# Performance work log

Measured on AMD Instinct MI355X. Metric: run time of the kernel, lower is better.

## Reference

```python
import jax, jax.numpy as jnp
import numpy as np

EPS = 1e-5
B, NA, T, D, H, L, DFF, E = 4, 64, 128, 128, 8, 3, 512, 65536
NN = T * NA  # nodes per graph = t*n after reshape(b, t*n, f)
DH = D // H


def _layer_norm(x, g, b):
    m = x.mean(-1, keepdims=True)
    v = ((x - m) ** 2).mean(-1, keepdims=True)
    return (x - m) * jax.lax.rsqrt(v + EPS) * g + b


def _pos_encoding(t, d):
    pos = jnp.arange(t, dtype=jnp.float32)[:, None]
    i = jnp.arange(0, d, 2, dtype=jnp.float32)
    ang = pos * jnp.exp(-jnp.log(10000.0) * i / d)
    pe = jnp.zeros((t, d), jnp.float32)
    return pe.at[:, 0::2].set(jnp.sin(ang)).at[:, 1::2].set(jnp.cos(ang))


def _forward(all_hist_feat, edge_weight, hist_w, hist_b,
             attn_wq, attn_bq, attn_wk, attn_bk, attn_wv, attn_bv, attn_wo, attn_bo,
             ln1_g, ln1_b, ff_w1, ff_b1, ff_w2, ff_b2, ln2_g, ln2_b,
             bn_g, bn_b, lin_graph_w, lin_graph_b, edge_index):
    b, n, t, _ = all_hist_feat.shape
    # history embedding: Linear(3, D)  -> [b, n, t, D]
    x = all_hist_feat @ hist_w + hist_b
    # sinusoidal positional encoding over the time axis
    out_e = x + _pos_encoding(t, D)
    scale = 1.0 / jnp.sqrt(jnp.asarray(DH, jnp.float32))
    for l in range(L):  # small fixed layer count
        q = out_e @ attn_wq[l] + attn_bq[l]
        k = out_e @ attn_wk[l] + attn_bk[l]
        v = out_e @ attn_wv[l] + attn_bv[l]
        qh = q.reshape(b, n, t, H, DH)
        kh = k.reshape(b, n, t, H, DH)
        vh = v.reshape(b, n, t, H, DH)
        scores = jnp.einsum('bnqhd,bnkhd->bnhqk', qh, kh) * scale
        attn = jax.nn.softmax(scores, axis=-1)
        o = jnp.einsum('bnhqk,bnkhd->bnqhd', attn, vh).reshape(b, n, t, D)
        o = o @ attn_wo[l] + attn_bo[l]
        h1 = _layer_norm(out_e + o, ln1_g[l], ln1_b[l])
        ff = jax.nn.relu(h1 @ ff_w1[l] + ff_b1[l]) @ ff_w2[l] + ff_b2[l]
        out_e = _layer_norm(h1 + ff, ln2_g[l], ln2_b[l])
    # graph stage: nodes are (time, agent) pairs, index = time*n + agent
    graph_w = out_e.transpose(0, 2, 1, 3).reshape(b, t * n, D)
    graph_x = x.transpose(0, 2, 1, 3).reshape(b, t * n, D)
    # GCNConv_Fixed_W (no self loops, no normalize): per-node score then
    # edge-weighted scatter-add from source to target (PyG convention)
    s = (graph_w * graph_x).sum(-1)  # [b, t*n]
    src, dst = edge_index[:, 0], edge_index[:, 1]

    def agg(s_b, src_b, dst_b, ew_b):
        return jax.ops.segment_sum(ew_b * s_b[src_b], dst_b, num_segments=NN)

    graph_out = jax.vmap(agg)(s, src, dst, edge_weight)  # [b, t*n]
    g = graph_out.reshape(b, t, n)
    # BatchNorm2d(1) on [b, 1, n, t]: single channel -> global batch stats
    m = g.mean()
    var = g.var()
    g = (g - m) * jax.lax.rsqrt(var + EPS) * bn_g[0] + bn_b[0]
    g4 = g.transpose(0, 2, 1)[..., None]  # [b, n, t, 1]
    return g4 @ lin_graph_w + lin_graph_b  # [b, n, t, D]


def setup_inputs() -> dict:
    keys = iter(jax.random.split(jax.random.key(0), 64))

    def nrm(shape, scale):
        return jax.random.normal(next(keys), shape, jnp.float32) * scale

    inp = {
        'all_hist_feat': nrm((B, NA, T, 3), 1.0),
        'edge_index': jax.random.randint(next(keys), (B, 2, E), 0, NN, jnp.int32),
        'edge_weight': jax.random.uniform(next(keys), (B, E), jnp.float32),
        'hist_w': nrm((3, D), 0.5), 'hist_b': nrm((D,), 0.02),
        'attn_wq': nrm((L, D, D), D ** -0.5), 'attn_bq': jnp.zeros((L, D)),
        'attn_wk': nrm((L, D, D), D ** -0.5), 'attn_bk': jnp.zeros((L, D)),
        'attn_wv': nrm((L, D, D), D ** -0.5), 'attn_bv': jnp.zeros((L, D)),
        'attn_wo': nrm((L, D, D), D ** -0.5), 'attn_bo': jnp.zeros((L, D)),
        'ln1_g': jnp.ones((L, D)), 'ln1_b': jnp.zeros((L, D)),
        'ff_w1': nrm((L, D, DFF), D ** -0.5), 'ff_b1': jnp.zeros((L, DFF)),
        'ff_w2': nrm((L, DFF, D), DFF ** -0.5), 'ff_b2': jnp.zeros((L, D)),
        'ln2_g': jnp.ones((L, D)), 'ln2_b': jnp.zeros((L, D)),
        'bn_g': jnp.ones((1,)), 'bn_b': jnp.zeros((1,)),
        'lin_graph_w': nrm((1, D), 1.0), 'lin_graph_b': jnp.zeros((D,)),
    }
    return inp


def reference(all_hist_feat, edge_index, edge_weight, hist_w, hist_b,
              attn_wq, attn_bq, attn_wk, attn_bk, attn_wv, attn_bv, attn_wo, attn_bo,
              ln1_g, ln1_b, ff_w1, ff_b1, ff_w2, ff_b2, ln2_g, ln2_b,
              bn_g, bn_b, lin_graph_w, lin_graph_b):
    return _forward(all_hist_feat, edge_weight, hist_w, hist_b,
                    attn_wq, attn_bq, attn_wk, attn_bk, attn_wv, attn_bv, attn_wo, attn_bo,
                    ln1_g, ln1_b, ff_w1, ff_b1, ff_w2, ff_b2, ln2_g, ln2_b,
                    bn_g, bn_b, lin_graph_w, lin_graph_b, edge_index)
```

## Files before the change

### kernel.cpp

```cpp
#include <hip/hip_runtime.h>
#include <hip/hip_bf16.h>
#include <math.h>

#define EPS_ 1e-5f
constexpr int B_ = 4, NA = 64, T_ = 128, D_ = 128, H_ = 8, L_ = 3, DFF = 512, E_ = 65536;
constexpr int DH = D_ / H_;
constexpr int NN = T_ * NA;
constexpr int NTOT = B_ * NA * T_;
constexpr int QLD = 384;
constexpr size_t NE_ = (size_t)NTOT * D_;

typedef __bf16 bf16x8 __attribute__((ext_vector_type(8)));
typedef float f32x4 __attribute__((ext_vector_type(4)));

__global__ __launch_bounds__(256) void embed_kernel(
    const float* __restrict__ hist, const float* __restrict__ w,
    const float* __restrict__ b, float* __restrict__ x, float* __restrict__ e) {
  int idx = blockIdx.x * 256 + threadIdx.x;
  if (idx >= NTOT * D_) return;
  int d = idx & (D_ - 1);
  int r = idx >> 7;
  int t = r & (T_ - 1);
  const float* hp = hist + (size_t)r * 3;
  float acc = b[d];
  acc += hp[0] * w[0 * D_ + d];
  acc += hp[1] * w[1 * D_ + d];
  acc += hp[2] * w[2 * D_ + d];
  x[idx] = acc;
  int p = d >> 1;
  float ang = (float)t * expf(-logf(10000.f) * (2.f * (float)p) / (float)D_);
  float pe = (d & 1) ? cosf(ang) : sinf(ang);
  e[idx] = acc + pe;
}

__global__ __launch_bounds__(256) void convert_weights(
    const float* __restrict__ wq, const float* __restrict__ wk,
    const float* __restrict__ wv, const float* __restrict__ wo,
    const float* __restrict__ w1, const float* __restrict__ w2,
    __bf16* __restrict__ hi, __bf16* __restrict__ lo) {
  const int LW = 196608;
  int idx = blockIdx.x * 256 + threadIdx.x;
  if (idx >= L_ * LW) return;
  int l = idx / LW;
  int rem = idx - l * LW;
  float src;
  int n, k, K, segoff;
  if (rem < 49152) {
    n = rem >> 7; k = rem & 127; K = 128; segoff = 0;
    int which = n >> 7, nl = n & 127;
    const float* W = (which == 0) ? wq : (which == 1) ? wk : wv;
    src = W[(size_t)l * 16384 + k * 128 + nl];
  } else if (rem < 65536) {
    int r2 = rem - 49152;
    n = r2 >> 7; k = r2 & 127; K = 128; segoff = 49152;
    src = wo[(size_t)l * 16384 + k * 128 + n];
  } else if (rem < 131072) {
    int r2 = rem - 65536;
    n = r2 >> 7; k = r2 & 127; K = 128; segoff = 65536;
    src = w1[(size_t)l * 65536 + k * 512 + n];
  } else {
    int r2 = rem - 131072;
    n = r2 >> 9; k = r2 & 511; K = 512; segoff = 131072;
    src = w2[(size_t)l * 65536 + k * 128 + n];
  }
  int nt = n >> 4, kt = k >> 5;
  int lane = ((k >> 3) & 3) * 16 + (n & 15);
  int j = k & 7;
  int dst = l * LW + segoff + ((nt * (K / 32) + kt) * 64 + lane) * 8 + j;
  __bf16 h = (__bf16)src;
  hi[dst] = h;
  lo[dst] = (__bf16)(src - (float)h);
}

__global__ __launch_bounds__(256) void bias_pack(
    const float* __restrict__ bq, const float* __restrict__ bk,
    const float* __restrict__ bv, float* __restrict__ pb) {
  int idx = blockIdx.x * 256 + threadIdx.x;
  if (idx >= L_ * QLD) return;
  int l = idx / QLD, n = idx - l * QLD;
  int which = n >> 7, nl = n & 127;
  const float* src = (which == 0) ? bq : (which == 1) ? bk : bv;
  pb[idx] = src[l * 128 + nl];
}

__device__ __forceinline__ void split8(const float* __restrict__ p,
                                       bf16x8& hi, bf16x8& lo) {
  float4 x0 = *(const float4*)p;
  float4 x1 = *(const float4*)(p + 4);
  float xv[8] = {x0.x, x0.y, x0.z, x0.w, x1.x, x1.y, x1.z, x1.w};
#pragma unroll
  for (int j = 0; j < 8; ++j) {
    __bf16 h = (__bf16)xv[j];
    hi[j] = h;
    lo[j] = (__bf16)(xv[j] - (float)h);
  }
}

__device__ __forceinline__ void cvt8(const float4& x0, const float4& x1,
                                     bf16x8& hi, bf16x8& lo) {
  float xv[8] = {x0.x, x0.y, x0.z, x0.w, x1.x, x1.y, x1.z, x1.w};
#pragma unroll
  for (int j = 0; j < 8; ++j) {
    __bf16 h = (__bf16)xv[j];
    hi[j] = h;
    lo[j] = (__bf16)(xv[j] - (float)h);
  }
}

#define GB_LOADA(buf, kt)                                                                  \
  {                                                                                        \
    _Pragma("unroll") for (int mf_ = 0; mf_ < 4; ++mf_) {                                  \
      const float* p_ = A + (size_t)(row0 + mf_ * 16 + m16) * lda + (kt) * 32 + quad * 8;  \
      ar[buf][mf_][0] = *(const float4*)p_;                                                \
      ar[buf][mf_][1] = *(const float4*)(p_ + 4);                                          \
    }                                                                                      \
  }
#define GB_LOADW(buf, kt)                                                                  \
  {                                                                                        \
    _Pragma("unroll") for (int nf_ = 0; nf_ < 4; ++nf_) {                                  \
      size_t off_ = ((size_t)(ctb + nf_) * (K / 32) + (kt)) * 512 + lane * 8;              \
      bh[buf][nf_] = *(const bf16x8*)(Whi + off_);                                         \
      bl[buf][nf_] = *(const bf16x8*)(Wlo + off_);                                         \
    }                                                                                      \
  }

template <int EPI, int K>
__global__ __launch_bounds__(256) void gemm_big(
    const float* __restrict__ A, int lda,
    const __bf16* __restrict__ Whi, const __bf16* __restrict__ Wlo,
    const float* __restrict__ bias,
    float* __restrict__ C, int ldc) {
  const int wave = threadIdx.x >> 6;
  const int lane = threadIdx.x & 63;
  const int m16 = lane & 15;
  const int quad = lane >> 4;
  const int wrow = wave >> 1, wcol = wave & 1;
  const int row0 = blockIdx.y * 128 + wrow * 64;
  const int col0 = blockIdx.x * 128 + wcol * 64;
  const int ctb = col0 >> 4;

  f32x4 acc[4][4] = {};
  float4 ar[2][4][2];
  bf16x8 bh[2][4], bl[2][4];
  GB_LOADA(0, 0);
  GB_LOADW(0, 0);
#pragma unroll
  for (int kt = 0; kt < K / 32; ++kt) {
    const int cur = kt & 1, nxt = cur ^ 1;
    if (kt < K / 32 - 1) {
      GB_LOADA(nxt, kt + 1);
      GB_LOADW(nxt, kt + 1);
    }
    bf16x8 ahi[4], alo[4];
#pragma unroll
    for (int mf = 0; mf < 4; ++mf)
      cvt8(ar[cur][mf][0], ar[cur][mf][1], ahi[mf], alo[mf]);
#pragma unroll
    for (int mf = 0; mf < 4; ++mf)
#pragma unroll
      for (int nf = 0; nf < 4; ++nf) {
        acc[mf][nf] = __builtin_amdgcn_mfma_f32_16x16x32_bf16(ahi[mf], bh[cur][nf], acc[mf][nf], 0, 0, 0);
        acc[mf][nf] = __builtin_amdgcn_mfma_f32_16x16x32_bf16(ahi[mf], bl[cur][nf], acc[mf][nf], 0, 0, 0);
        acc[mf][nf] = __builtin_amdgcn_mfma_f32_16x16x32_bf16(alo[mf], bh[cur][nf], acc[mf][nf], 0, 0, 0);
      }
  }
#pragma unroll
  for (int mf = 0; mf < 4; ++mf)
#pragma unroll
    for (int nf = 0; nf < 4; ++nf) {
      int c = col0 + nf * 16 + m16;
      float bj = bias[c];
#pragma unroll
      for (int reg = 0; reg < 4; ++reg) {
        int r = row0 + mf * 16 + quad * 4 + reg;
        float v = acc[mf][nf][reg] + bj;
        if (EPI == 1) v = fmaxf(v, 0.f);
        C[(size_t)r * ldc + c] = v;
      }
    }
}
#undef GB_LOADA
#undef GB_LOADW

template <int K>
__global__ __launch_bounds__(256) void gemm_ln(
    const float* __restrict__ A, int lda,
    const __bf16* __restrict__ Whi, const __bf16* __restrict__ Wlo,
    const float* __restrict__ bias, const float* __restrict__ resid,
    const float* __restrict__ lng, const float* __restrict__ lnb,
    float* __restrict__ C) {
  const int wave = threadIdx.x >> 6;
  const int lane = threadIdx.x & 63;
  const int m16 = lane & 15;
  const int quad = lane >> 4;
  const int wrow = wave >> 1, wcol = wave & 1;
  const int row0 = blockIdx.y * 64 + wrow * 32;
  const int col0 = wcol * 64;
  const int ctb = wcol * 4;

  f32x4 acc[2][4] = {};
#pragma unroll
  for (int k0 = 0; k0 < K; k0 += 32) {
    bf16x8 ahi[2], alo[2];
#pragma unroll
    for (int mf = 0; mf < 2; ++mf)
      split8(A + (size_t)(row0 + mf * 16 + m16) * lda + k0 + quad * 8, ahi[mf], alo[mf]);
    bf16x8 bhi[4], blo[4];
#pragma unroll
    for (int nf = 0; nf < 4; ++nf) {
      size_t off = ((size_t)(ctb + nf) * (K / 32) + (k0 >> 5)) * 512 + lane * 8;
      bhi[nf] = *(const bf16x8*)(Whi + off);
      blo[nf] = *(const bf16x8*)(Wlo + off);
    }
#pragma unroll
    for (int mf = 0; mf < 2; ++mf)
#pragma unroll
      for (int nf = 0; nf < 4; ++nf) {
        acc[mf][nf] = __builtin_amdgcn_mfma_f32_16x16x32_bf16(ahi[mf], bhi[nf], acc[mf][nf], 0, 0, 0);
        acc[mf][nf] = __builtin_amdgcn_mfma_f32_16x16x32_bf16(ahi[mf], blo[nf], acc[mf][nf], 0, 0, 0);
        acc[mf][nf] = __builtin_amdgcn_mfma_f32_16x16x32_bf16(alo[mf], bhi[nf], acc[mf][nf], 0, 0, 0);
      }
  }
  __shared__ float rs[64][2], rq[64][2];
#pragma unroll
  for (int mf = 0; mf < 2; ++mf)
#pragma unroll
    for (int reg = 0; reg < 4; ++reg) {
      int lr = wrow * 32 + mf * 16 + quad * 4 + reg;
      int gr = blockIdx.y * 64 + lr;
      float s = 0.f, qq = 0.f;
#pragma unroll
      for (int nf = 0; nf < 4; ++nf) {
        int c = col0 + nf * 16 + m16;
        float v = acc[mf][nf][reg] + bias[c] + resid[(size_t)gr * 128 + c];
        acc[mf][nf][reg] = v;
        s += v;
        qq += v * v;
      }
#pragma unroll
      for (int off = 1; off < 16; off <<= 1) {
        s += __shfl_xor(s, off, 64);
        qq += __shfl_xor(qq, off, 64);
      }
      if (m16 == 0) { rs[lr][wcol] = s; rq[lr][wcol] = qq; }
    }
  __syncthreads();
#pragma unroll
  for (int mf = 0; mf < 2; ++mf)
#pragma unroll
    for (int reg = 0; reg < 4; ++reg) {
      int lr = wrow * 32 + mf * 16 + quad * 4 + reg;
      int gr = blockIdx.y * 64 + lr;
      float mean = (rs[lr][0] + rs[lr][1]) * (1.f / 128.f);
      float var = (rq[lr][0] + rq[lr][1]) * (1.f / 128.f) - mean * mean;
      float rstd = rsqrtf(var + EPS_);
#pragma unroll
      for (int nf = 0; nf < 4; ++nf) {
        int c = col0 + nf * 16 + m16;
        C[(size_t)gr * 128 + c] = (acc[mf][nf][reg] - mean) * rstd * lng[c] + lnb[c];
      }
    }
}

#define FF1_LOADA(buf, kt)                                                                  \
  {                                                                                         \
    _Pragma("unroll") for (int mf_ = 0; mf_ < 2; ++mf_) {                                   \
      const float* p_ = A + (size_t)(grow0 + mf_ * 16 + m16) * 128 + (kt) * 32 + quad * 8;  \
      ar[buf][mf_][0] = *(const float4*)p_;                                                 \
      ar[buf][mf_][1] = *(const float4*)(p_ + 4);                                           \
    }                                                                                       \
  }
#define FF1_LOADW(buf, kt)                                                                  \
  {                                                                                         \
    _Pragma("unroll") for (int nf_ = 0; nf_ < 8; ++nf_) {                                   \
      size_t off_ = ((size_t)(wave * 8 + nf_) * 4 + (kt)) * 512 + lane * 8;                 \
      bh[buf][nf_] = *(const bf16x8*)(W1hi + off_);                                         \
      bl[buf][nf_] = *(const bf16x8*)(W1lo + off_);                                         \
    }                                                                                       \
  }
#define FF2_LOADW(buf, kt)                                                                  \
  {                                                                                         \
    _Pragma("unroll") for (int nf_ = 0; nf_ < 2; ++nf_) {                                   \
      size_t off_ = ((size_t)(wave * 2 + nf_) * 16 + (kt)) * 512 + lane * 8;                \
      wh[buf][nf_] = *(const bf16x8*)(W2hi + off_);                                         \
      wl[buf][nf_] = *(const bf16x8*)(W2lo + off_);                                         \
    }                                                                                       \
  }

template <int SDOT>
__global__ __launch_bounds__(256) void ff_fused(
    const float* __restrict__ A,
    const __bf16* __restrict__ W1hi, const __bf16* __restrict__ W1lo,
    const float* __restrict__ b1v,
    const __bf16* __restrict__ W2hi, const __bf16* __restrict__ W2lo,
    const float* __restrict__ b2v, const float* __restrict__ resid,
    const float* __restrict__ lng, const float* __restrict__ lnb,
    float* __restrict__ C,
    const float* __restrict__ bx, float* __restrict__ sdst) {
  extern __shared__ float Amid[];
  const int wave = threadIdx.x >> 6;
  const int lane = threadIdx.x & 63;
  const int m16 = lane & 15;
  const int quad = lane >> 4;
  const int grow0 = blockIdx.x * 32;

  {
    f32x4 acc[2][8] = {};
    float4 ar[2][2][2];
    bf16x8 bh[2][8], bl[2][8];
    FF1_LOADA(0, 0);
    FF1_LOADW(0, 0);
#pragma unroll
    for (int kt = 0; kt < 4; ++kt) {
      const int cur = kt & 1, nxt = cur ^ 1;
      if (kt < 3) {
        FF1_LOADA(nxt, kt + 1);
        FF1_LOADW(nxt, kt + 1);
      }
      bf16x8 ahi[2], alo[2];
#pragma unroll
      for (int mf = 0; mf < 2; ++mf)
        cvt8(ar[cur][mf][0], ar[cur][mf][1], ahi[mf], alo[mf]);
#pragma unroll
      for (int nf = 0; nf < 8; ++nf)
#pragma unroll
        for (int mf = 0; mf < 2; ++mf) {
          acc[mf][nf] = __builtin_amdgcn_mfma_f32_16x16x32_bf16(ahi[mf], bh[cur][nf], acc[mf][nf], 0, 0, 0);
          acc[mf][nf] = __builtin_amdgcn_mfma_f32_16x16x32_bf16(ahi[mf], bl[cur][nf], acc[mf][nf], 0, 0, 0);
          acc[mf][nf] = __builtin_amdgcn_mfma_f32_16x16x32_bf16(alo[mf], bh[cur][nf], acc[mf][nf], 0, 0, 0);
        }
    }
#pragma unroll
    for (int mf = 0; mf < 2; ++mf)
#pragma unroll
      for (int nf = 0; nf < 8; ++nf) {
        int c = wave * 128 + nf * 16 + m16;
        float bj = b1v[c];
#pragma unroll
        for (int reg = 0; reg < 4; ++reg) {
          int r = mf * 16 + quad * 4 + reg;
          Amid[r * 513 + c] = fmaxf(acc[mf][nf][reg] + bj, 0.f);
        }
      }
  }
  __syncthreads();

  f32x4 acc2[2][2] = {};
  {
    bf16x8 wh[2][2], wl[2][2];
    FF2_LOADW(0, 0);
#pragma unroll
    for (int kt = 0; kt < 16; ++kt) {
      const int cur = kt & 1;
      if (kt < 15) FF2_LOADW(cur ^ 1, kt + 1);
      bf16x8 ahi[2], alo[2];
#pragma unroll
      for (int mf = 0; mf < 2; ++mf)
        split8(&Amid[(mf * 16 + m16) * 513 + kt * 32 + quad * 8], ahi[mf], alo[mf]);
#pragma unroll
      for (int mf = 0; mf < 2; ++mf)
#pragma unroll
        for (int nf = 0; nf < 2; ++nf) {
          acc2[mf][nf] = __builtin_amdgcn_mfma_f32_16x16x32_bf16(ahi[mf], wh[cur][nf], acc2[mf][nf], 0, 0, 0);
          acc2[mf][nf] = __builtin_amdgcn_mfma_f32_16x16x32_bf16(ahi[mf], wl[cur][nf], acc2[mf][nf], 0, 0, 0);
          acc2[mf][nf] = __builtin_amdgcn_mfma_f32_16x16x32_bf16(alo[mf], wh[cur][nf], acc2[mf][nf], 0, 0, 0);
        }
    }
  }

  __shared__ float rs[32][4], rq[32][4], sd[32][4];
  const int col0 = wave * 32;
#pragma unroll
  for (int mf = 0; mf < 2; ++mf)
#pragma unroll
    for (int reg = 0; reg < 4; ++reg) {
      int lr = mf * 16 + quad * 4 + reg;
      int gr = grow0 + lr;
      float s = 0.f, qq = 0.f;
#pragma unroll
      for (int nf = 0; nf < 2; ++nf) {
        int c = col0 + nf * 16 + m16;
        float v = acc2[mf][nf][reg] + b2v[c] + resid[(size_t)gr * 128 + c];
        acc2[mf][nf][reg] = v;
        s += v;
        qq += v * v;
      }
#pragma unroll
      for (int off = 1; off < 16; off <<= 1) {
        s += __shfl_xor(s, off, 64);
        qq += __shfl_xor(qq, off, 64);
      }
      if (m16 == 0) { rs[lr][wave] = s; rq[lr][wave] = qq; }
    }
  __syncthreads();
#pragma unroll
  for (int mf = 0; mf < 2; ++mf)
#pragma unroll
    for (int reg = 0; reg < 4; ++reg) {
      int lr = mf * 16 + quad * 4 + reg;
      int gr = grow0 + lr;
      float mean = (rs[lr][0] + rs[lr][1] + rs[lr][2] + rs[lr][3]) * (1.f / 128.f);
      float var = (rq[lr][0] + rq[lr][1] + rq[lr][2] + rq[lr][3]) * (1.f / 128.f) - mean * mean;
      float rstd = rsqrtf(var + EPS_);
      float sdp = 0.f;
#pragma unroll
      for (int nf = 0; nf < 2; ++nf) {
        int c = col0 + nf * 16 + m16;
        float v = (acc2[mf][nf][reg] - mean) * rstd * lng[c] + lnb[c];
        C[(size_t)gr * 128 + c] = v;
        if (SDOT) sdp += v * bx[(size_t)gr * 128 + c];
      }
      if (SDOT) {
#pragma unroll
        for (int off = 1; off < 16; off <<= 1) sdp += __shfl_xor(sdp, off, 64);
        if (m16 == 0) sd[lr][wave] = sdp;
      }
    }
  if (SDOT) {
    __syncthreads();
    if (threadIdx.x < 32) {
      int lr = threadIdx.x;
      int gr = grow0 + lr;
      float sv = sd[lr][0] + sd[lr][1] + sd[lr][2] + sd[lr][3];
      int t = gr & (T_ - 1);
      int bn = gr >> 7;
      int n = bn & (NA - 1);
      int b = bn >> 6;
      sdst[(size_t)b * NN + t * NA + n] = sv;
    }
  }
}
#undef FF1_LOADA
#undef FF1_LOADW
#undef FF2_LOADW

__global__ __launch_bounds__(256) void attn_mfma(float* __restrict__ qkv) {
  const int h = blockIdx.x & (H_ - 1);
  const int bn = blockIdx.x >> 3;
  const int wave = threadIdx.x >> 6;
  const int lane = threadIdx.x & 63;
  const int m16 = lane & 15;
  const int quad = lane >> 4;
  const int row0 = wave * 32;
  const float* Qb = qkv + (size_t)bn * T_ * QLD + h * DH;
  const float* Kb = Qb + 128;
  const float* Vb = Qb + 256;
  float* Ob = (float*)Vb;

  __shared__ __bf16 Plds[4][32][136];
  __shared__ __bf16 KH[8][32][8], KL[8][32][8];
  __shared__ __bf16 VH[4][64][8], VL[4][64][8];

  for (int u = threadIdx.x; u < 1024; u += 256) {
    int isV = u >> 9;
    int r2 = u & 511;
    int t = r2 >> 2, c4 = r2 & 3;
    float4 v = *(const float4*)((isV ? Vb : Kb) + (size_t)t * QLD + c4 * 4);
    float xv[4] = {v.x, v.y, v.z, v.w};
#pragma unroll
    for (int i = 0; i < 4; ++i) {
      int dh = c4 * 4 + i;
      __bf16 hh = (__bf16)xv[i];
      __bf16 ll = (__bf16)(xv[i] - (float)hh);
      if (isV) {
        int kc = t >> 5, rem = t & 31;
        int vl = (rem >> 3) * 16 + dh;
        VH[kc][vl][rem & 7] = hh;
        VL[kc][vl][rem & 7] = ll;
      } else {
        int nf = t >> 4;
        int kl = (dh >> 3) * 16 + (t & 15);
        KH[nf][kl][dh & 7] = hh;
        KL[nf][kl][dh & 7] = ll;
      }
    }
  }

  bf16x8 qhi[2], qlo[2];
#pragma unroll
  for (int mf = 0; mf < 2; ++mf) {
    if (quad < 2) {
      split8(Qb + (size_t)(row0 + mf * 16 + m16) * QLD + quad * 8, qhi[mf], qlo[mf]);
    } else {
#pragma unroll
      for (int j = 0; j < 8; ++j) { qhi[mf][j] = (__bf16)0.f; qlo[mf][j] = (__bf16)0.f; }
    }
  }
  __syncthreads();

  f32x4 acc[2][8] = {};
#pragma unroll
  for (int nf = 0; nf < 8; ++nf) {
    bf16x8 khi, klo;
    if (quad < 2) {
      khi = *(const bf16x8*)&KH[nf][lane][0];
      klo = *(const bf16x8*)&KL[nf][lane][0];
    } else {
#pragma unroll
      for (int j = 0; j < 8; ++j) { khi[j] = (__bf16)0.f; klo[j] = (__bf16)0.f; }
    }
#pragma unroll
    for (int mf = 0; mf < 2; ++mf) {
      acc[mf][nf] = __builtin_amdgcn_mfma_f32_16x16x32_bf16(qhi[mf], khi, acc[mf][nf], 0, 0, 0);
      acc[mf][nf] = __builtin_amdgcn_mfma_f32_16x16x32_bf16(qhi[mf], klo, acc[mf][nf], 0, 0, 0);
      acc[mf][nf] = __builtin_amdgcn_mfma_f32_16x16x32_bf16(qlo[mf], khi, acc[mf][nf], 0, 0, 0);
    }
  }

  const float scale = 0.25f;
#pragma unroll
  for (int mf = 0; mf < 2; ++mf)
#pragma unroll
    for (int reg = 0; reg < 4; ++reg) {
      float mx = -1e30f;
#pragma unroll
      for (int nf = 0; nf < 8; ++nf) mx = fmaxf(mx, acc[mf][nf][reg]);
#pragma unroll
      for (int off = 1; off < 16; off <<= 1) mx = fmaxf(mx, __shfl_xor(mx, off, 64));
      float sum = 0.f;
#pragma unroll
      for (int nf = 0; nf < 8; ++nf) {
        float e = __expf((acc[mf][nf][reg] - mx) * scale);
        acc[mf][nf][reg] = e;
        sum += e;
      }
#pragma unroll
      for (int off = 1; off < 16; off <<= 1) sum += __shfl_xor(sum, off, 64);
      float inv = 1.f / sum;
#pragma unroll
      for (int nf = 0; nf < 8; ++nf) acc[mf][nf][reg] *= inv;
    }

#pragma unroll
  for (int mf = 0; mf < 2; ++mf)
#pragma unroll
    for (int nf = 0; nf < 8; ++nf)
#pragma unroll
      for (int reg = 0; reg < 4; ++reg)
        Plds[wave][mf * 16 + quad * 4 + reg][nf * 16 + m16] = (__bf16)acc[mf][nf][reg];

  f32x4 oacc[2] = {};
#pragma unroll
  for (int kc = 0; kc < 4; ++kc) {
    bf16x8 pa0 = *(const bf16x8*)&Plds[wave][m16][kc * 32 + quad * 8];
    bf16x8 pa1 = *(const bf16x8*)&Plds[wave][16 + m16][kc * 32 + quad * 8];
    bf16x8 vhi = *(const bf16x8*)&VH[kc][lane][0];
    bf16x8 vlo = *(const bf16x8*)&VL[kc][lane][0];
    oacc[0] = __builtin_amdgcn_mfma_f32_16x16x32_bf16(pa0, vhi, oacc[0], 0, 0, 0);
    oacc[0] = __builtin_amdgcn_mfma_f32_16x16x32_bf16(pa0, vlo, oacc[0], 0, 0, 0);
    oacc[1] = __builtin_amdgcn_mfma_f32_16x16x32_bf16(pa1, vhi, oacc[1], 0, 0, 0);
    oacc[1] = __builtin_amdgcn_mfma_f32_16x16x32_bf16(pa1, vlo, oacc[1], 0, 0, 0);
  }

#pragma unroll
  for (int mf = 0; mf < 2; ++mf)
#pragma unroll
    for (int reg = 0; reg < 4; ++reg) {
      int r = row0 + mf * 16 + quad * 4 + reg;
      Ob[(size_t)r * QLD + m16] = oacc[mf][reg];
    }
}

__global__ __launch_bounds__(256) void scatter_kernel(
    const float* __restrict__ s, const int* __restrict__ ei,
    const float* __restrict__ ew, float* __restrict__ g) {
  int idx = blockIdx.x * 256 + threadIdx.x;
  if (idx >= B_ * E_) return;
  int b = idx >> 16;
  int e = idx & (E_ - 1);
  int src = ei[(size_t)b * 2 * E_ + e];
  int dst = ei[(size_t)b * 2 * E_ + E_ + e];
  float w = ew[(size_t)b * E_ + e];
  atomicAdd(&g[(size_t)b * NN + dst], w * s[(size_t)b * NN + src]);
}

__global__ __launch_bounds__(256) void stats_partial(
    const float* __restrict__ g, float* __restrict__ st) {
  int i = blockIdx.x * 256 + threadIdx.x;
  float v = g[i];
  float sum = v, sq = v * v;
#pragma unroll
  for (int off = 32; off; off >>= 1) {
    sum += __shfl_down(sum, off, 64);
    sq += __shfl_down(sq, off, 64);
  }
  __shared__ float s1[4], s2[4];
  int w = threadIdx.x >> 6;
  if ((threadIdx.x & 63) == 0) { s1[w] = sum; s2[w] = sq; }
  __syncthreads();
  if (threadIdx.x == 0) {
    atomicAdd(&st[0], s1[0] + s1[1] + s1[2] + s1[3]);
    atomicAdd(&st[1], s2[0] + s2[1] + s2[2] + s2[3]);
  }
}

__global__ __launch_bounds__(256) void final_kernel(
    const float* __restrict__ g, const float* __restrict__ st,
    const float* __restrict__ bng, const float* __restrict__ bnb,
    const float* __restrict__ lw, const float* __restrict__ lb,
    float* __restrict__ out) {
  int idx = blockIdx.x * 256 + threadIdx.x;
  if (idx >= NTOT * D_) return;
  int d = idx & (D_ - 1);
  int r = idx >> 7;
  int t = r & (T_ - 1);
  int bn = r >> 7;
  int n = bn & (NA - 1);
  int b = bn >> 6;
  const float invn = 1.f / (float)(B_ * NN);
  float m = st[0] * invn;
  float var = st[1] * invn - m * m;
  float rs = rsqrtf(var + EPS_);
  float gv = g[(size_t)b * NN + t * NA + n];
  float val = (gv - m) * rs * bng[0] + bnb[0];
  out[idx] = val * lw[d] + lb[d];
}

extern "C" void kernel_launch(void* const* d_in, const int* in_sizes, int n_in,
                              void* d_out, int out_size, void* d_ws, size_t ws_size,
                              hipStream_t stream) {
  const float* hist = (const float*)d_in[0];
  const int* eidx = (const int*)d_in[1];
  const float* ew = (const float*)d_in[2];
  const float* hw = (const float*)d_in[3];
  const float* hb = (const float*)d_in[4];
  const float* wq = (const float*)d_in[5];
  const float* bq = (const float*)d_in[6];
  const float* wk = (const float*)d_in[7];
  const float* bk = (const float*)d_in[8];
  const float* wv = (const float*)d_in[9];
  const float* bv = (const float*)d_in[10];
  const float* wo = (const float*)d_in[11];
  const float* bo = (const float*)d_in[12];
  const float* ln1g = (const float*)d_in[13];
  const float* ln1b = (const float*)d_in[14];
  const float* w1 = (const float*)d_in[15];
  const float* b1 = (const float*)d_in[16];
  const float* w2 = (const float*)d_in[17];
  const float* b2 = (const float*)d_in[18];
  const float* ln2g = (const float*)d_in[19];
  const float* ln2b = (const float*)d_in[20];
  const float* bng = (const float*)d_in[21];
  const float* bnb = (const float*)d_in[22];
  const float* lgw = (const float*)d_in[23];
  const float* lgb = (const float*)d_in[24];
  float* out = (float*)d_out;

  float* ws = (float*)d_ws;
  const size_t NE = NE_;
  float* bx = ws + 0 * NE;
  float* be = ws + 1 * NE;
  float* h1 = ws + 2 * NE;
  float* qkv = ws + 3 * NE;
  float* bs_ = ws + 7 * NE;
  float* bg_ = bs_ + NTOT;
  float* bst = bg_ + NTOT;
  float* pbias = bst + 2;
  const int LW = 196608;
  __bf16* whiB = (__bf16*)(pbias + L_ * QLD);
  __bf16* wloB = whiB + (size_t)L_ * LW;

  const size_t ffshm = (size_t)32 * 513 * sizeof(float);
  static bool ff_attr_done = false;
  if (!ff_attr_done) {
    (void)hipFuncSetAttribute(reinterpret_cast<const void*>(&ff_fused<0>),
                              hipFuncAttributeMaxDynamicSharedMemorySize, (int)ffshm);
    (void)hipFuncSetAttribute(reinterpret_cast<const void*>(&ff_fused<1>),
                              hipFuncAttributeMaxDynamicSharedMemorySize, (int)ffshm);
    ff_attr_done = true;
  }

  convert_weights<<<(L_ * LW + 255) / 256, 256, 0, stream>>>(
      wq, wk, wv, wo, w1, w2, whiB, wloB);
  bias_pack<<<(L_ * QLD + 255) / 256, 256, 0, stream>>>(bq, bk, bv, pbias);
  embed_kernel<<<(NTOT * D_) / 256, 256, 0, stream>>>(hist, hw, hb, bx, be);

  for (int l = 0; l < L_; ++l) {
    const __bf16* hiL = whiB + (size_t)l * LW;
    const __bf16* loL = wloB + (size_t)l * LW;
    gemm_big<0, 128><<<dim3(3, NTOT / 128), 256, 0, stream>>>(
        be, 128, hiL, loL, pbias + l * QLD, qkv, QLD);
    attn_mfma<<<B_ * NA * H_, 256, 0, stream>>>(qkv);
    gemm_ln<128><<<dim3(1, NTOT / 64), 256, 0, stream>>>(
        qkv + 256, QLD, hiL + 49152, loL + 49152, bo + l * D_, be,
        ln1g + l * D_, ln1b + l * D_, h1);
    if (l < L_ - 1) {
      ff_fused<0><<<NTOT / 32, 256, ffshm, stream>>>(
          h1, hiL + 65536, loL + 65536, b1 + l * DFF,
          hiL + 131072, loL + 131072, b2 + l * D_, h1,
          ln2g + l * D_, ln2b + l * D_, be, nullptr, nullptr);
    } else {
      ff_fused<1><<<NTOT / 32, 256, ffshm, stream>>>(
          h1, hiL + 65536, loL + 65536, b1 + l * DFF,
          hiL + 131072, loL + 131072, b2 + l * D_, h1,
          ln2g + l * D_, ln2b + l * D_, be, bx, bs_);
    }
  }

  hipMemsetAsync(bg_, 0, ((size_t)B_ * NN + 2) * sizeof(float), stream);
  scatter_kernel<<<(B_ * E_) / 256, 256, 0, stream>>>(bs_, eidx, ew, bg_);
  stats_partial<<<(B_ * NN) / 256, 256, 0, stream>>>(bg_, bst);
  final_kernel<<<(NTOT * D_) / 256, 256, 0, stream>>>(bg_, bst, bng, bnb, lgw, lgb, out);
}
```

Measured before the change: 550.2 us.

## Retile fused FFN to 64-row blocks with 8 waves and pre-split bf16 intermediate

The fused feed-forward kernel now processes 64 rows per block with 512 threads (8 waves). Each wave owns 64 hidden columns in the first GEMM and 16 output columns in the second, so each weight fragment is reused across more rows. The ReLU intermediate is stored in shared memory already split into packed bf16 hi/lo pairs, which removes the repeated fp32-to-bf16 splitting during the second GEMM. The A-operand loads are no longer double-buffered, and the larger shared-memory footprint per block may lower occupancy.

```diff
diff --git a/kernel.cpp b/kernel.cpp
--- a/kernel.cpp
+++ b/kernel.cpp
@@ -11,6 +11,7 @@
 constexpr size_t NE_ = (size_t)NTOT * D_;
 
 typedef __bf16 bf16x8 __attribute__((ext_vector_type(8)));
+typedef __bf16 bf16x2 __attribute__((ext_vector_type(2)));
 typedef float f32x4 __attribute__((ext_vector_type(4)));
 
 __global__ __launch_bounds__(256) void embed_kernel(
@@ -107,6 +108,26 @@
   }
 }
 
+__device__ __forceinline__ unsigned pack_hl(float v) {
+  __bf16 h = (__bf16)v;
+  __bf16 l = (__bf16)(v - (float)h);
+  bf16x2 p;
+  p[0] = h;
+  p[1] = l;
+  return __builtin_bit_cast(unsigned, p);
+}
+
+__device__ __forceinline__ void unpack8(const uint4& a, const uint4& b,
+                                        bf16x8& hi, bf16x8& lo) {
+  unsigned w[8] = {a.x, a.y, a.z, a.w, b.x, b.y, b.z, b.w};
+#pragma unroll
+  for (int j = 0; j < 8; ++j) {
+    bf16x2 p = __builtin_bit_cast(bf16x2, w[j]);
+    hi[j] = p[0];
+    lo[j] = p[1];
+  }
+}
+
 #define GB_LOADA(buf, kt)                                                                  \
   {                                                                                        \
     _Pragma("unroll") for (int mf_ = 0; mf_ < 4; ++mf_) {                                  \
@@ -262,33 +283,23 @@
     }
 }
 
-#define FF1_LOADA(buf, kt)                                                                  \
-  {                                                                                         \
-    _Pragma("unroll") for (int mf_ = 0; mf_ < 2; ++mf_) {                                   \
-      const float* p_ = A + (size_t)(grow0 + mf_ * 16 + m16) * 128 + (kt) * 32 + quad * 8;  \
-      ar[buf][mf_][0] = *(const float4*)p_;                                                 \
-      ar[buf][mf_][1] = *(const float4*)(p_ + 4);                                           \
-    }                                                                                       \
-  }
 #define FF1_LOADW(buf, kt)                                                                  \
   {                                                                                         \
-    _Pragma("unroll") for (int nf_ = 0; nf_ < 8; ++nf_) {                                   \
-      size_t off_ = ((size_t)(wave * 8 + nf_) * 4 + (kt)) * 512 + lane * 8;                 \
+    _Pragma("unroll") for (int nf_ = 0; nf_ < 4; ++nf_) {                                   \
+      size_t off_ = ((size_t)(wave * 4 + nf_) * 4 + (kt)) * 512 + lane * 8;                 \
       bh[buf][nf_] = *(const bf16x8*)(W1hi + off_);                                         \
       bl[buf][nf_] = *(const bf16x8*)(W1lo + off_);                                         \
     }                                                                                       \
   }
 #define FF2_LOADW(buf, kt)                                                                  \
   {                                                                                         \
-    _Pragma("unroll") for (int nf_ = 0; nf_ < 2; ++nf_) {                                   \
-      size_t off_ = ((size_t)(wave * 2 + nf_) * 16 + (kt)) * 512 + lane * 8;                \
-      wh[buf][nf_] = *(const bf16x8*)(W2hi + off_);                                         \
-      wl[buf][nf_] = *(const bf16x8*)(W2lo + off_);                                         \
-    }                                                                                       \
+    size_t off_ = ((size_t)wave * 16 + (kt)) * 512 + lane * 8;                              \
+    wh[buf] = *(const bf16x8*)(W2hi + off_);                                                \
+    wl[buf] = *(const bf16x8*)(W2lo + off_);                                                \
   }
 
 template <int SDOT>
-__global__ __launch_bounds__(256) void ff_fused(
+__global__ __launch_bounds__(512) void ff_fused(
     const float* __restrict__ A,
     const __bf16* __restrict__ W1hi, const __bf16* __restrict__ W1lo,
     const float* __restrict__ b1v,
@@ -297,94 +308,82 @@
     const float* __restrict__ lng, const float* __restrict__ lnb,
     float* __restrict__ C,
     const float* __restrict__ bx, float* __restrict__ sdst) {
-  extern __shared__ float Amid[];
+  extern __shared__ unsigned AmidU[];
   const int wave = threadIdx.x >> 6;
   const int lane = threadIdx.x & 63;
   const int m16 = lane & 15;
   const int quad = lane >> 4;
-  const int grow0 = blockIdx.x * 32;
+  const int grow0 = blockIdx.x * 64;
 
   {
-    f32x4 acc[2][8] = {};
-    float4 ar[2][2][2];
-    bf16x8 bh[2][8], bl[2][8];
-    FF1_LOADA(0, 0);
+    f32x4 acc[4][4] = {};
+    bf16x8 bh[2][4], bl[2][4];
     FF1_LOADW(0, 0);
 #pragma unroll
     for (int kt = 0; kt < 4; ++kt) {
-      const int cur = kt & 1, nxt = cur ^ 1;
-      if (kt < 3) {
-        FF1_LOADA(nxt, kt + 1);
-        FF1_LOADW(nxt, kt + 1);
-      }
-      bf16x8 ahi[2], alo[2];
-#pragma unroll
-      for (int mf = 0; mf < 2; ++mf)
-        cvt8(ar[cur][mf][0], ar[cur][mf][1], ahi[mf], alo[mf]);
-#pragma unroll
-      for (int nf = 0; nf < 8; ++nf)
-#pragma unroll
-        for (int mf = 0; mf < 2; ++mf) {
+      const int cur = kt & 1;
+      if (kt < 3) FF1_LOADW(cur ^ 1, kt + 1);
+      bf16x8 ahi[4], alo[4];
+#pragma unroll
+      for (int mf = 0; mf < 4; ++mf)
+        split8(A + (size_t)(grow0 + mf * 16 + m16) * 128 + kt * 32 + quad * 8, ahi[mf], alo[mf]);
+#pragma unroll
+      for (int mf = 0; mf < 4; ++mf)
+#pragma unroll
+        for (int nf = 0; nf < 4; ++nf) {
           acc[mf][nf] = __builtin_amdgcn_mfma_f32_16x16x32_bf16(ahi[mf], bh[cur][nf], acc[mf][nf], 0, 0, 0);
           acc[mf][nf] = __builtin_amdgcn_mfma_f32_16x16x32_bf16(ahi[mf], bl[cur][nf], acc[mf][nf], 0, 0, 0);
           acc[mf][nf] = __builtin_amdgcn_mfma_f32_16x16x32_bf16(alo[mf], bh[cur][nf], acc[mf][nf], 0, 0, 0);
         }
     }
 #pragma unroll
-    for (int mf = 0; mf < 2; ++mf)
-#pragma unroll
-      for (int nf = 0; nf < 8; ++nf) {
-        int c = wave * 128 + nf * 16 + m16;
+    for (int mf = 0; mf < 4; ++mf)
+#pragma unroll
+      for (int nf = 0; nf < 4; ++nf) {
+        int c = wave * 64 + nf * 16 + m16;
         float bj = b1v[c];
 #pragma unroll
         for (int reg = 0; reg < 4; ++reg) {
           int r = mf * 16 + quad * 4 + reg;
-          Amid[r * 513 + c] = fmaxf(acc[mf][nf][reg] + bj, 0.f);
+          AmidU[r * 513 + c] = pack_hl(fmaxf(acc[mf][nf][reg] + bj, 0.f));
         }
       }
   }
   __syncthreads();
 
-  f32x4 acc2[2][2] = {};
+  f32x4 acc2[4] = {};
   {
-    bf16x8 wh[2][2], wl[2][2];
+    bf16x8 wh[2], wl[2];
     FF2_LOADW(0, 0);
 #pragma unroll
     for (int kt = 0; kt < 16; ++kt) {
       const int cur = kt & 1;
       if (kt < 15) FF2_LOADW(cur ^ 1, kt + 1);
-      bf16x8 ahi[2], alo[2];
-#pragma unroll
-      for (int mf = 0; mf < 2; ++mf)
-        split8(&Amid[(mf * 16 + m16) * 513 + kt * 32 + quad * 8], ahi[mf], alo[mf]);
-#pragma unroll
-      for (int mf = 0; mf < 2; ++mf)
-#pragma unroll
-        for (int nf = 0; nf < 2; ++nf) {
-          acc2[mf][nf] = __builtin_amdgcn_mfma_f32_16x16x32_bf16(ahi[mf], wh[cur][nf], acc2[mf][nf], 0, 0, 0);
-          acc2[mf][nf] = __builtin_amdgcn_mfma_f32_16x16x32_bf16(ahi[mf], wl[cur][nf], acc2[mf][nf], 0, 0, 0);
-          acc2[mf][nf] = __builtin_amdgcn_mfma_f32_16x16x32_bf16(alo[mf], wh[cur][nf], acc2[mf][nf], 0, 0, 0);
-        }
-    }
-  }
-
-  __shared__ float rs[32][4], rq[32][4], sd[32][4];
-  const int col0 = wave * 32;
-#pragma unroll
-  for (int mf = 0; mf < 2; ++mf)
+#pragma unroll
+      for (int mf = 0; mf < 4; ++mf) {
+        const unsigned* p = &AmidU[(mf * 16 + m16) * 513 + kt * 32 + quad * 8];
+        uint4 w0 = *(const uint4*)p;
+        uint4 w1v = *(const uint4*)(p + 4);
+        bf16x8 ahi, alo;
+        unpack8(w0, w1v, ahi, alo);
+        acc2[mf] = __builtin_amdgcn_mfma_f32_16x16x32_bf16(ahi, wh[cur], acc2[mf], 0, 0, 0);
+        acc2[mf] = __builtin_amdgcn_mfma_f32_16x16x32_bf16(ahi, wl[cur], acc2[mf], 0, 0, 0);
+        acc2[mf] = __builtin_amdgcn_mfma_f32_16x16x32_bf16(alo, wh[cur], acc2[mf], 0, 0, 0);
+      }
+    }
+  }
+
+  __shared__ float rs[64][8], rq[64][8], sd[64][8];
+  const int c = wave * 16 + m16;
+#pragma unroll
+  for (int mf = 0; mf < 4; ++mf)
 #pragma unroll
     for (int reg = 0; reg < 4; ++reg) {
       int lr = mf * 16 + quad * 4 + reg;
       int gr = grow0 + lr;
-      float s = 0.f, qq = 0.f;
-#pragma unroll
-      for (int nf = 0; nf < 2; ++nf) {
-        int c = col0 + nf * 16 + m16;
-        float v = acc2[mf][nf][reg] + b2v[c] + resid[(size_t)gr * 128 + c];
-        acc2[mf][nf][reg] = v;
-        s += v;
-        qq += v * v;
-      }
+      float v = acc2[mf][reg] + b2v[c] + resid[(size_t)gr * 128 + c];
+      acc2[mf][reg] = v;
+      float s = v, qq = v * v;
 #pragma unroll
       for (int off = 1; off < 16; off <<= 1) {
         s += __shfl_xor(s, off, 64);
@@ -394,23 +393,21 @@
     }
   __syncthreads();
 #pragma unroll
-  for (int mf = 0; mf < 2; ++mf)
+  for (int mf = 0; mf < 4; ++mf)
 #pragma unroll
     for (int reg = 0; reg < 4; ++reg) {
       int lr = mf * 16 + quad * 4 + reg;
       int gr = grow0 + lr;
-      float mean = (rs[lr][0] + rs[lr][1] + rs[lr][2] + rs[lr][3]) * (1.f / 128.f);
-      float var = (rq[lr][0] + rq[lr][1] + rq[lr][2] + rq[lr][3]) * (1.f / 128.f) - mean * mean;
+      float sm = 0.f, sq = 0.f;
+#pragma unroll
+      for (int wv = 0; wv < 8; ++wv) { sm += rs[lr][wv]; sq += rq[lr][wv]; }
+      float mean = sm * (1.f / 128.f);
+      float var = sq * (1.f / 128.f) - mean * mean;
       float rstd = rsqrtf(var + EPS_);
-      float sdp = 0.f;
-#pragma unroll
-      for (int nf = 0; nf < 2; ++nf) {
-        int c = col0 + nf * 16 + m16;
-        float v = (acc2[mf][nf][reg] - mean) * rstd * lng[c] + lnb[c];
-        C[(size_t)gr * 128 + c] = v;
-        if (SDOT) sdp += v * bx[(size_t)gr * 128 + c];
-      }
+      float v = (acc2[mf][reg] - mean) * rstd * lng[c] + lnb[c];
+      C[(size_t)gr * 128 + c] = v;
       if (SDOT) {
+        float sdp = v * bx[(size_t)gr * 128 + c];
 #pragma unroll
         for (int off = 1; off < 16; off <<= 1) sdp += __shfl_xor(sdp, off, 64);
         if (m16 == 0) sd[lr][wave] = sdp;
@@ -418,10 +415,12 @@
     }
   if (SDOT) {
     __syncthreads();
-    if (threadIdx.x < 32) {
+    if (threadIdx.x < 64) {
       int lr = threadIdx.x;
       int gr = grow0 + lr;
-      float sv = sd[lr][0] + sd[lr][1] + sd[lr][2] + sd[lr][3];
+      float sv = 0.f;
+#pragma unroll
+      for (int wv = 0; wv < 8; ++wv) sv += sd[lr][wv];
       int t = gr & (T_ - 1);
       int bn = gr >> 7;
       int n = bn & (NA - 1);
@@ -430,7 +429,6 @@
     }
   }
 }
-#undef FF1_LOADA
 #undef FF1_LOADW
 #undef FF2_LOADW
 
@@ -660,7 +658,7 @@
   __bf16* whiB = (__bf16*)(pbias + L_ * QLD);
   __bf16* wloB = whiB + (size_t)L_ * LW;
 
-  const size_t ffshm = (size_t)32 * 513 * sizeof(float);
+  const size_t ffshm = (size_t)64 * 513 * sizeof(unsigned);
   static bool ff_attr_done = false;
   if (!ff_attr_done) {
     (void)hipFuncSetAttribute(reinterpret_cast<const void*>(&ff_fused<0>),
@@ -685,12 +683,12 @@
         qkv + 256, QLD, hiL + 49152, loL + 49152, bo + l * D_, be,
         ln1g + l * D_, ln1b + l * D_, h1);
     if (l < L_ - 1) {
-      ff_fused<0><<<NTOT / 32, 256, ffshm, stream>>>(
+      ff_fused<0><<<NTOT / 64, 512, ffshm, stream>>>(
           h1, hiL + 65536, loL + 65536, b1 + l * DFF,
           hiL + 131072, loL + 131072, b2 + l * D_, h1,
           ln2g + l * D_, ln2b + l * D_, be, nullptr, nullptr);
     } else {
-      ff_fused<1><<<NTOT / 32, 256, ffshm, stream>>>(
+      ff_fused<1><<<NTOT / 64, 512, ffshm, stream>>>(
           h1, hiL + 65536, loL + 65536, b1 + l * DFF,
           hiL + 131072, loL + 131072, b2 + l * D_, h1,
           ln2g + l * D_, ln2b + l * D_, be, bx, bs_);
```

Result: slower. 652.3 us (+18.6%).
